# Performance work log

Measured on AMD Instinct MI355X. Metric: run time of the kernel, lower is better.

## Reference

```python
import jax, jax.numpy as jnp
import numpy as np

B, S, D, H = 2, 2048, 1024, 16
DK = D // H


def setup_inputs() -> dict:
    key = jax.random.key(0)
    ks = jax.random.split(key, 7)
    x = jax.random.normal(ks[0], (B, S, D), dtype=jnp.float32)
    gamma = jax.random.normal(ks[1], (D,), dtype=jnp.float32)
    mask = jax.random.randint(ks[2], (B, S), 0, 2, dtype=jnp.int32)
    w_qkv_w = jax.random.normal(ks[3], (D, 3 * D), dtype=jnp.float32) / np.sqrt(D)
    w_qkv_b = jax.random.normal(ks[4], (3 * D,), dtype=jnp.float32) * 0.02
    w_o_w = jax.random.normal(ks[5], (D, D), dtype=jnp.float32) / np.sqrt(D)
    w_o_b = jax.random.normal(ks[6], (D,), dtype=jnp.float32) * 0.02
    return {"x": x, "gamma": gamma, "mask": mask, "w_qkv_w": w_qkv_w,
            "w_qkv_b": w_qkv_b, "w_o_w": w_o_w, "w_o_b": w_o_b}


def reference(x, gamma, mask, w_qkv_w, w_qkv_b, w_o_w, w_o_b):
    b, s, d = x.shape
    # QKV projection, then per-head interleaved chunk (matches torch view+chunk)
    qkv = x @ w_qkv_w + w_qkv_b                      # [B,S,3D]
    qkv = qkv.reshape(b, s, H, 3 * DK).transpose(0, 2, 1, 3)  # [B,H,S,3*dk]
    q, k, v = jnp.split(qkv, 3, axis=-1)             # each [B,H,S,dk]
    scale = 1.0 / np.sqrt(DK).astype(np.float32)
    scores = jnp.einsum('bhqd,bhkd->bhqk', q, k) * scale  # [B,H,S,S]
    m = mask[:, None, None, :]                       # 2D mask -> [B,1,1,S]
    scores = jnp.where(m == 0, -jnp.inf, scores)
    attn = jax.nn.softmax(scores, axis=-1)           # dropout p=0.0 -> identity
    out = jnp.einsum('bhqk,bhkd->bhqd', attn, v)     # [B,H,S,dk]
    out = out.transpose(0, 2, 1, 3).reshape(b, s, d) # [B,S,D]
    out = out @ w_o_w + w_o_b
    return (gamma + 1.0) * out
```

## Files before the change

### kernel.cpp

```cpp
#include <hip/hip_runtime.h>
#include <hip/hip_bf16.h>


using bf16 = __hip_bfloat16;
typedef __attribute__((ext_vector_type(8))) short bf16x8;
typedef __attribute__((ext_vector_type(4))) float f32x4;

#define QSCALE 0.18033688011112042f

static __device__ __forceinline__ f32x4 mfma_bf16(bf16x8 a, bf16x8 b, f32x4 c) {
    return __builtin_amdgcn_mfma_f32_16x16x32_bf16(a, b, c, 0, 0, 0);
}

static __device__ __forceinline__ void gld_lds16(const void* g, void* s) {
    __builtin_amdgcn_global_load_lds(
        (const __attribute__((address_space(1))) unsigned int*)g,
        (__attribute__((address_space(3))) unsigned int*)s,
        16, 0, 0);
}

static __device__ __forceinline__ short f2s(float f) {
    bf16 h = __float2bfloat16(f);
    return *reinterpret_cast<short*>(&h);
}

__global__ void prep_kernel(const float* __restrict__ x, bf16* __restrict__ xb,
                            const float* __restrict__ wqkv, bf16* __restrict__ wqkvT,
                            const float* __restrict__ wo, bf16* __restrict__ woT) {
    __shared__ float tile[32][33];
    int blk = blockIdx.x;
    if (blk < 4096) {
        int i = blk * 256 + threadIdx.x;
        float4 f = reinterpret_cast<const float4*>(x)[i];
        xb[4*i+0] = __float2bfloat16(f.x);
        xb[4*i+1] = __float2bfloat16(f.y);
        xb[4*i+2] = __float2bfloat16(f.z);
        xb[4*i+3] = __float2bfloat16(f.w);
        return;
    }
    const float* in; bf16* out; int R, C, bx, by;
    if (blk < 7168) {
        int idx = blk - 4096; in = wqkv; out = wqkvT; R = 1024; C = 3072;
        bx = idx % 96; by = idx / 96;
    } else {
        int idx = blk - 7168; in = wo; out = woT; R = 1024; C = 1024;
        bx = idx & 31; by = idx >> 5;
    }
    int c0 = bx * 32, r0 = by * 32;
    int xo = threadIdx.x & 31, yo = threadIdx.x >> 5;
#pragma unroll
    for (int i = 0; i < 32; i += 8) tile[yo + i][xo] = in[(size_t)(r0 + yo + i) * C + c0 + xo];
    __syncthreads();
#pragma unroll
    for (int i = 0; i < 32; i += 8)
        out[(size_t)(c0 + yo + i) * R + r0 + xo] = __float2bfloat16(tile[xo][yo + i]);
}

template <int TM, int MINW>
__global__ __launch_bounds__(256, MINW)
void gemm_bt_kernel(const bf16* __restrict__ A, const bf16* __restrict__ Bt,
                    int M, int N, int K,
                    const float* __restrict__ bias,
                    bf16* __restrict__ Qout, bf16* __restrict__ Kout, bf16* __restrict__ Vout) {
    constexpr int MI = TM / 32;
    constexpr int CA = TM / 32;
    __shared__ __align__(16) bf16 As[TM * 64];
    __shared__ __align__(16) bf16 Bs[128 * 64];

    const int tid  = threadIdx.x;
    const int wave = tid >> 6, lane = tid & 63;
    const int quad = lane >> 4, l16 = lane & 15;
    const int wr = wave >> 1, wc = wave & 1;
    const int bm = blockIdx.y, bn = blockIdx.x;

    f32x4 acc[MI][4] = {};

    const int crow = lane >> 3;
    const int sblk = (lane & 7) ^ (crow & 7);
    const bf16* gA[CA]; const bf16* gB[4]; bf16* lA[CA]; bf16* lB[4];
#pragma unroll
    for (int c = 0; c < CA; ++c) {
        int ch = wave * CA + c;
        gA[c] = A + (size_t)(bm * TM + ch * 8 + crow) * K + sblk * 8;
        lA[c] = As + ch * 512 + lane * 8;
    }
#pragma unroll
    for (int c = 0; c < 4; ++c) {
        int ch = wave * 4 + c;
        gB[c] = Bt + (size_t)(bn * 128 + ch * 8 + crow) * K + sblk * 8;
        lB[c] = Bs + ch * 512 + lane * 8;
    }
    const int xr = l16 & 7;

    for (int k0 = 0; k0 < K; k0 += 64) {
#pragma unroll
        for (int c = 0; c < CA; ++c) gld_lds16(gA[c] + k0, lA[c]);
#pragma unroll
        for (int c = 0; c < 4; ++c) gld_lds16(gB[c] + k0, lB[c]);
        __syncthreads();
#pragma unroll
        for (int ks = 0; ks < 2; ++ks) {
            bf16x8 af[MI], bfr[4];
#pragma unroll
            for (int mi = 0; mi < MI; ++mi)
                af[mi] = *(const bf16x8*)(As + (wr * (TM/2) + mi * 16 + l16) * 64 + ((4 * ks + quad) ^ xr) * 8);
#pragma unroll
            for (int ni = 0; ni < 4; ++ni)
                bfr[ni] = *(const bf16x8*)(Bs + (wc * 64 + ni * 16 + l16) * 64 + ((4 * ks + quad) ^ xr) * 8);
#pragma unroll
            for (int mi = 0; mi < MI; ++mi)
#pragma unroll
                for (int ni = 0; ni < 4; ++ni)
                    acc[mi][ni] = mfma_bf16(af[mi], bfr[ni], acc[mi][ni]);
        }
        __syncthreads();
    }

#pragma unroll
    for (int mi = 0; mi < MI; ++mi) {
#pragma unroll
        for (int ni = 0; ni < 4; ++ni) {
            const int col = bn * 128 + wc * 64 + ni * 16 + l16;
            const int row0 = bm * TM + wr * (TM/2) + mi * 16 + quad * 4;
            const float bs = bias[col];
            float vv[4];
#pragma unroll
            for (int r = 0; r < 4; ++r) vv[r] = acc[mi][ni][r] + bs;
            const int h = col / 192;
            const int rr = col - h * 192;
            const int which = rr >> 6, dk = rr & 63;
            const int b = row0 >> 11, s0 = row0 & 2047;
            const size_t bh = (size_t)b * 16 + h;
            if (which == 0) {
#pragma unroll
                for (int r = 0; r < 4; ++r)
                    Qout[(bh * 2048 + s0 + r) * 64 + dk] = __float2bfloat16(vv[r] * QSCALE);
            } else if (which == 1) {
#pragma unroll
                for (int r = 0; r < 4; ++r)
                    Kout[(bh * 2048 + s0 + r) * 64 + dk] = __float2bfloat16(vv[r]);
            } else {
                const int sp0 = (s0 & ~31) | ((s0 & 12) << 1) | ((s0 & 16) >> 2);
                short4 pv;
                pv.x = f2s(vv[0]); pv.y = f2s(vv[1]);
                pv.z = f2s(vv[2]); pv.w = f2s(vv[3]);
                *reinterpret_cast<short4*>(&Vout[(bh * 64 + dk) * 2048 + sp0]) = pv;
            }
        }
    }
}

__global__ __launch_bounds__(512, 2)
void gemm_out_kernel(const bf16* __restrict__ A, const bf16* __restrict__ Bt,
                     const float* __restrict__ bias, const float* __restrict__ gamma,
                     float* __restrict__ Cout) {
    constexpr int K = 1024, N = 1024;
    __shared__ __align__(16) bf16 As[128 * 64];
    __shared__ __align__(16) bf16 Bs[128 * 64];

    const int tid = threadIdx.x;
    const int wave = tid >> 6, lane = tid & 63;
    const int quad = lane >> 4, l16 = lane & 15;
    const int wr = wave >> 1, wc = wave & 1;

    const int lid = blockIdx.x + (blockIdx.y << 3);
    const int w = (lid & 7) * 32 + (lid >> 3);
    const int bm = w >> 3, bn = w & 7;

    f32x4 acc[2][4] = {};

    const int crow = lane >> 3;
    const int sblk = (lane & 7) ^ (crow & 7);
    const bf16* gA[2]; const bf16* gB[2]; bf16* lA[2]; bf16* lB[2];
#pragma unroll
    for (int c = 0; c < 2; ++c) {
        int ch = wave * 2 + c;
        gA[c] = A + (size_t)(bm * 128 + ch * 8 + crow) * K + sblk * 8;
        lA[c] = As + ch * 512 + lane * 8;
        gB[c] = Bt + (size_t)(bn * 128 + ch * 8 + crow) * K + sblk * 8;
        lB[c] = Bs + ch * 512 + lane * 8;
    }
    const int xr = l16 & 7;

    for (int k0 = 0; k0 < K; k0 += 64) {
#pragma unroll
        for (int c = 0; c < 2; ++c) {
            gld_lds16(gA[c] + k0, lA[c]);
            gld_lds16(gB[c] + k0, lB[c]);
        }
        __syncthreads();
#pragma unroll
        for (int ks = 0; ks < 2; ++ks) {
            bf16x8 af[2], bfr[4];
#pragma unroll
            for (int mi = 0; mi < 2; ++mi)
                af[mi] = *(const bf16x8*)(As + (wr * 32 + mi * 16 + l16) * 64 + ((4 * ks + quad) ^ xr) * 8);
#pragma unroll
            for (int ni = 0; ni < 4; ++ni)
                bfr[ni] = *(const bf16x8*)(Bs + (wc * 64 + ni * 16 + l16) * 64 + ((4 * ks + quad) ^ xr) * 8);
#pragma unroll
            for (int mi = 0; mi < 2; ++mi)
#pragma unroll
                for (int ni = 0; ni < 4; ++ni)
                    acc[mi][ni] = mfma_bf16(af[mi], bfr[ni], acc[mi][ni]);
        }
        __syncthreads();
    }

#pragma unroll
    for (int mi = 0; mi < 2; ++mi)
#pragma unroll
        for (int ni = 0; ni < 4; ++ni) {
            const int col = bn * 128 + wc * 64 + ni * 16 + l16;
            const int row0 = bm * 128 + wr * 32 + mi * 16 + quad * 4;
            const float bs = bias[col];
            const float gm = gamma[col] + 1.0f;
#pragma unroll
            for (int r = 0; r < 4; ++r)
                Cout[(size_t)(row0 + r) * N + col] = gm * (acc[mi][ni][r] + bs);
        }
}

__global__ __launch_bounds__(256, 2)
void attn_kernel(const bf16* __restrict__ Qb, const bf16* __restrict__ Kb,
                 const bf16* __restrict__ Vtp, const int* __restrict__ mask,
                 bf16* __restrict__ Aout) {
    __shared__ __align__(16) bf16 Ks[2][2][4096];
    __shared__ __align__(16) bf16 Vs[2][2][4096];
    __shared__ float Biass[2][2][64];

    const int lid = blockIdx.x + (blockIdx.y << 4);
    const int w   = (lid & 7) * 64 + (lid >> 3);
    const int bh  = w >> 4;
    const int b = bh >> 4, h = bh & 15;
    const int q0 = (w & 15) * 128;
    const int tid = threadIdx.x;
    const int wave = tid >> 6, lane = tid & 63;
    const int qg = wave >> 1, kg = wave & 1;
    const int quad = lane >> 4, l16 = lane & 15;
    const int xr = l16 & 7;

    bf16x8 aq[4][2];
#pragma unroll
    for (int m = 0; m < 4; ++m) {
        const bf16* qp = Qb + ((size_t)bh * 2048 + q0 + qg * 64 + m * 16 + l16) * 64;
        aq[m][0] = *(const bf16x8*)(qp + quad * 8);
        aq[m][1] = *(const bf16x8*)(qp + 32 + quad * 8);
    }

    bf16x8 ones;
#pragma unroll
    for (int j = 0; j < 8; ++j) ones[j] = (short)0x3F80;

    f32x4 O[4][4] = {};
    f32x4 Lacc[4] = {};

    const int r8 = lane >> 3, b8 = lane & 7;
    const int srcb = b8 ^ r8;
    const bf16* gK = Kb  + ((size_t)bh * 2048 + wave * 8 + r8) * 64 + srcb * 8;
    const bf16* gV = Vtp + ((size_t)bh * 64 + wave * 8 + r8) * 2048 + srcb * 8;
    const int so = wave * 512 + lane * 8;

    int mreg = 0;
#pragma unroll
    for (int ti = 0; ti < 2; ++ti)
#pragma unroll
        for (int c = 0; c < 2; ++c) {
            gld_lds16(gK + (size_t)ti * 4096 + c * 2048, &Ks[0][ti][c * 2048 + so]);
            gld_lds16(gV + (size_t)ti * 64 + c * 65536, &Vs[0][ti][c * 2048 + so]);
        }
    if (tid < 128) {
        Biass[0][tid >> 6][tid & 63] = mask[b * 2048 + tid] ? -24.0f : -1e30f;
        mreg = mask[b * 2048 + 128 + tid];
    }

    for (int t = 0; t < 16; ++t) {
        __syncthreads();
        const int cur = t & 1, nxt = cur ^ 1;

        if (t < 15) {
            const int u0 = 2 * t + 2;
#pragma unroll
            for (int ti = 0; ti < 2; ++ti)
#pragma unroll
                for (int c = 0; c < 2; ++c) {
                    gld_lds16(gK + (size_t)(u0 + ti) * 4096 + c * 2048, &Ks[nxt][ti][c * 2048 + so]);
                    gld_lds16(gV + (size_t)(u0 + ti) * 64 + c * 65536, &Vs[nxt][ti][c * 2048 + so]);
                }
            if (tid < 128) Biass[nxt][tid >> 6][tid & 63] = mreg ? -24.0f : -1e30f;
        }
        if (t < 14 && tid < 128) mreg = mask[b * 2048 + t * 128 + 256 + tid];

        const bf16* kb = &Ks[cur][kg][0];
        const bf16* vb = &Vs[cur][kg][0];
        f32x4 bias4[4];
        bf16x8 bk[4][2];
#pragma unroll
        for (int kt4 = 0; kt4 < 4; ++kt4) {
            bias4[kt4] = *(const f32x4*)(&Biass[cur][kg][0] + kt4 * 16 + quad * 4);
            const bf16* kp2 = kb + (kt4 * 16 + l16) * 64;
            bk[kt4][0] = *(const bf16x8*)(kp2 + (quad ^ xr) * 8);
            bk[kt4][1] = *(const bf16x8*)(kp2 + ((quad + 4) ^ xr) * 8);
        }
        bf16x8 bv[2][4];
#pragma unroll
        for (int a = 0; a < 2; ++a)
#pragma unroll
            for (int nt = 0; nt < 4; ++nt)
                bv[a][nt] = *(const bf16x8*)(vb + (nt * 16 + l16) * 64 + ((a * 4 + quad) ^ xr) * 8);

        f32x4 sv0[2][4], sv1[2][4];
        __builtin_amdgcn_s_setprio(1);
#pragma unroll
        for (int mm = 0; mm < 2; ++mm)
#pragma unroll
            for (int kt4 = 0; kt4 < 4; ++kt4) {
                f32x4 c = mfma_bf16(bk[kt4][0], aq[mm][0], bias4[kt4]);
                sv0[mm][kt4] = mfma_bf16(bk[kt4][1], aq[mm][1], c);
            }

#pragma unroll
        for (int kt4 = 0; kt4 < 4; ++kt4) {
            f32x4 c0 = mfma_bf16(bk[kt4][0], aq[2][0], bias4[kt4]);
#pragma unroll
            for (int r = 0; r < 4; ++r)
                sv0[0][kt4][r] = __builtin_amdgcn_exp2f(sv0[0][kt4][r]);
            f32x4 c1 = mfma_bf16(bk[kt4][0], aq[3][0], bias4[kt4]);
#pragma unroll
            for (int r = 0; r < 4; ++r)
                sv0[1][kt4][r] = __builtin_amdgcn_exp2f(sv0[1][kt4][r]);
            sv1[0][kt4] = mfma_bf16(bk[kt4][1], aq[2][1], c0);
            sv1[1][kt4] = mfma_bf16(bk[kt4][1], aq[3][1], c1);
        }

#pragma unroll
        for (int mm = 0; mm < 2; ++mm) {
#pragma unroll
            for (int a = 0; a < 2; ++a) {
                bf16x8 pa;
                pa[0] = f2s(sv0[mm][2*a][0]);   pa[1] = f2s(sv0[mm][2*a][1]);
                pa[2] = f2s(sv0[mm][2*a][2]);   pa[3] = f2s(sv0[mm][2*a][3]);
                pa[4] = f2s(sv0[mm][2*a+1][0]); pa[5] = f2s(sv0[mm][2*a+1][1]);
                pa[6] = f2s(sv0[mm][2*a+1][2]); pa[7] = f2s(sv0[mm][2*a+1][3]);
                Lacc[mm] = mfma_bf16(pa, ones, Lacc[mm]);
#pragma unroll
                for (int nt = 0; nt < 4; ++nt)
                    O[mm][nt] = mfma_bf16(pa, bv[a][nt], O[mm][nt]);
#pragma unroll
                for (int r = 0; r < 4; ++r)
                    sv1[mm][2*a + (r >> 1)][(r & 1) + 2*((mm + a) & 1)] =
                        __builtin_amdgcn_exp2f(sv1[mm][2*a + (r >> 1)][(r & 1) + 2*((mm + a) & 1)]);
            }
        }
#pragma unroll
        for (int mm = 0; mm < 2; ++mm)
#pragma unroll
            for (int kt4 = 0; kt4 < 4; ++kt4)
#pragma unroll
                for (int r = 0; r < 4; ++r) {
                    if (((r >> 1) == 0 ? (2*((mm + (kt4 >> 1)) & 1)) : -1) == -1) {}
                }
#pragma unroll
        for (int mm = 0; mm < 2; ++mm)
#pragma unroll
            for (int a = 0; a < 2; ++a)
#pragma unroll
                for (int r = 0; r < 4; ++r) {
                    int kt4 = 2*a + (r >> 1);
                    int ri  = (r & 1) + 2*(((mm + a) & 1) ^ 1);
                    sv1[mm][kt4][ri] = __builtin_amdgcn_exp2f(sv1[mm][kt4][ri]);
                }

#pragma unroll
        for (int mm = 0; mm < 2; ++mm) {
            const int m = 2 + mm;
#pragma unroll
            for (int a = 0; a < 2; ++a) {
                bf16x8 pa;
                pa[0] = f2s(sv1[mm][2*a][0]);   pa[1] = f2s(sv1[mm][2*a][1]);
                pa[2] = f2s(sv1[mm][2*a][2]);   pa[3] = f2s(sv1[mm][2*a][3]);
                pa[4] = f2s(sv1[mm][2*a+1][0]); pa[5] = f2s(sv1[mm][2*a+1][1]);
                pa[6] = f2s(sv1[mm][2*a+1][2]); pa[7] = f2s(sv1[mm][2*a+1][3]);
                Lacc[m] = mfma_bf16(pa, ones, Lacc[m]);
#pragma unroll
                for (int nt = 0; nt < 4; ++nt)
                    O[m][nt] = mfma_bf16(pa, bv[a][nt], O[m][nt]);
            }
        }
        __builtin_amdgcn_s_setprio(0);
    }

    __syncthreads();
    float* cb = (float*)&Ks[0][0][0];
    float* lb = (float*)&Vs[0][0][0];
    if (kg == 1) {
#pragma unroll
        for (int m = 0; m < 4; ++m) {
#pragma unroll
            for (int nt = 0; nt < 4; ++nt)
#pragma unroll
                for (int r = 0; r < 4; ++r)
                    cb[qg * 4096 + (m * 16 + nt * 4 + r) * 64 + lane] = O[m][nt][r];
#pragma unroll
            for (int r = 0; r < 4; ++r)
                lb[qg * 1024 + (m * 4 + r) * 64 + lane] = Lacc[m][r];
        }
    }
    __syncthreads();
    if (kg == 0) {
#pragma unroll
        for (int m = 0; m < 4; ++m) {
            float inv[4];
#pragma unroll
            for (int r = 0; r < 4; ++r)
                inv[r] = __builtin_amdgcn_rcpf(Lacc[m][r] + lb[qg * 1024 + (m * 4 + r) * 64 + lane]);
#pragma unroll
            for (int nt = 0; nt < 4; ++nt)
#pragma unroll
                for (int r = 0; r < 4; ++r) {
                    int row = q0 + qg * 64 + m * 16 + quad * 4 + r;
                    float o = O[m][nt][r] + cb[qg * 4096 + (m * 16 + nt * 4 + r) * 64 + lane];
                    Aout[((size_t)b * 2048 + row) * 1024 + h * 64 + nt * 16 + l16] =
                        __float2bfloat16(o * inv[r]);
                }
        }
    }
}

extern "C" void kernel_launch(void* const* d_in, const int* in_sizes, int n_in,
                              void* d_out, int out_size, void* d_ws, size_t ws_size,
                              hipStream_t stream) {
    const float* x     = (const float*)d_in[0];
    const float* gamma = (const float*)d_in[1];
    const int*   mask  = (const int*)d_in[2];
    const float* wqkv  = (const float*)d_in[3];
    const float* bqkv  = (const float*)d_in[4];
    const float* wo    = (const float*)d_in[5];
    const float* bo    = (const float*)d_in[6];
    float* out = (float*)d_out;

    char* ws = (char*)d_ws;
    const size_t MB = 1u << 20;
    bf16* xb    = (bf16*)(ws);
    bf16* wqkvT = (bf16*)(ws + 8 * MB);
    bf16* woT   = (bf16*)(ws + 14 * MB);
    bf16* Qb    = (bf16*)(ws + 16 * MB);
    bf16* Kb    = (bf16*)(ws + 24 * MB);
    bf16* Vt    = (bf16*)(ws + 32 * MB);
    bf16* attn  = (bf16*)(ws + 40 * MB);

    prep_kernel<<<8192, 256, 0, stream>>>(x, xb, wqkv, wqkvT, wo, woT);

    gemm_bt_kernel<128, 3><<<dim3(24, 32), 256, 0, stream>>>(
        xb, wqkvT, 4096, 3072, 1024, bqkv, Qb, Kb, Vt);

    attn_kernel<<<dim3(16, 32), 256, 0, stream>>>(Qb, Kb, Vt, mask, attn);

    gemm_out_kernel<<<dim3(8, 32), 512, 0, stream>>>(attn, woT, bo, gamma, out);
}
```

Baseline: 180.2 us.

## Software-pipeline second-half softmax exp and PV MFMAs into the next iteration

The exp2, bf16 packing and P·V/row-sum MFMAs for query sub-tiles 2–3 move out of the current key-tile iteration. They now run at the start of the next iteration, interleaved with the QK MFMAs for sub-tiles 0–1, and an epilogue after the loop drains the last tile. This aims to overlap transcendental and conversion work with matrix-core work and cut the serialized tail of each iteration. In exchange, the score fragments and the V fragments must stay in registers across iterations, which raises register pressure and may lower occupancy or cause spills.

```diff
diff --git a/kernel.cpp b/kernel.cpp
--- a/kernel.cpp
+++ b/kernel.cpp
@@ -274,6 +274,9 @@
         mreg = mask[b * 2048 + 128 + tid];
     }
 
+    f32x4 sv1p[2][4];
+    bf16x8 bv[2][4];
+
     for (int t = 0; t < 16; ++t) {
         __syncthreads();
         const int cur = t & 1, nxt = cur ^ 1;
@@ -302,23 +305,56 @@
             bk[kt4][0] = *(const bf16x8*)(kp2 + (quad ^ xr) * 8);
             bk[kt4][1] = *(const bf16x8*)(kp2 + ((quad + 4) ^ xr) * 8);
         }
-        bf16x8 bv[2][4];
+
+        f32x4 sv0[2][4];
+        __builtin_amdgcn_s_setprio(1);
+        if (t > 0) {
+#pragma unroll
+            for (int kt4 = 0; kt4 < 4; ++kt4) {
+                f32x4 c0 = mfma_bf16(bk[kt4][0], aq[0][0], bias4[kt4]);
+#pragma unroll
+                for (int r = 0; r < 4; ++r)
+                    sv1p[0][kt4][r] = __builtin_amdgcn_exp2f(sv1p[0][kt4][r]);
+                f32x4 c1 = mfma_bf16(bk[kt4][0], aq[1][0], bias4[kt4]);
+#pragma unroll
+                for (int r = 0; r < 4; ++r)
+                    sv1p[1][kt4][r] = __builtin_amdgcn_exp2f(sv1p[1][kt4][r]);
+                sv0[0][kt4] = mfma_bf16(bk[kt4][1], aq[0][1], c0);
+                sv0[1][kt4] = mfma_bf16(bk[kt4][1], aq[1][1], c1);
+            }
+#pragma unroll
+            for (int mm = 0; mm < 2; ++mm) {
+#pragma unroll
+                for (int a = 0; a < 2; ++a) {
+                    bf16x8 pa;
+                    pa[0] = f2s(sv1p[mm][2*a][0]);   pa[1] = f2s(sv1p[mm][2*a][1]);
+                    pa[2] = f2s(sv1p[mm][2*a][2]);   pa[3] = f2s(sv1p[mm][2*a][3]);
+                    pa[4] = f2s(sv1p[mm][2*a+1][0]); pa[5] = f2s(sv1p[mm][2*a+1][1]);
+                    pa[6] = f2s(sv1p[mm][2*a+1][2]); pa[7] = f2s(sv1p[mm][2*a+1][3]);
+                    Lacc[2+mm] = mfma_bf16(pa, ones, Lacc[2+mm]);
+#pragma unroll
+                    for (int nt = 0; nt < 4; ++nt)
+                        O[2+mm][nt] = mfma_bf16(pa, bv[a][nt], O[2+mm][nt]);
+                }
+            }
+        } else {
+#pragma unroll
+            for (int kt4 = 0; kt4 < 4; ++kt4) {
+                f32x4 c0 = mfma_bf16(bk[kt4][0], aq[0][0], bias4[kt4]);
+                f32x4 c1 = mfma_bf16(bk[kt4][0], aq[1][0], bias4[kt4]);
+                sv0[0][kt4] = mfma_bf16(bk[kt4][1], aq[0][1], c0);
+                sv0[1][kt4] = mfma_bf16(bk[kt4][1], aq[1][1], c1);
+            }
+        }
+        __builtin_amdgcn_s_setprio(0);
+
 #pragma unroll
         for (int a = 0; a < 2; ++a)
 #pragma unroll
             for (int nt = 0; nt < 4; ++nt)
                 bv[a][nt] = *(const bf16x8*)(vb + (nt * 16 + l16) * 64 + ((a * 4 + quad) ^ xr) * 8);
 
-        f32x4 sv0[2][4], sv1[2][4];
         __builtin_amdgcn_s_setprio(1);
-#pragma unroll
-        for (int mm = 0; mm < 2; ++mm)
-#pragma unroll
-            for (int kt4 = 0; kt4 < 4; ++kt4) {
-                f32x4 c = mfma_bf16(bk[kt4][0], aq[mm][0], bias4[kt4]);
-                sv0[mm][kt4] = mfma_bf16(bk[kt4][1], aq[mm][1], c);
-            }
-
 #pragma unroll
         for (int kt4 = 0; kt4 < 4; ++kt4) {
             f32x4 c0 = mfma_bf16(bk[kt4][0], aq[2][0], bias4[kt4]);
@@ -329,10 +365,9 @@
 #pragma unroll
             for (int r = 0; r < 4; ++r)
                 sv0[1][kt4][r] = __builtin_amdgcn_exp2f(sv0[1][kt4][r]);
-            sv1[0][kt4] = mfma_bf16(bk[kt4][1], aq[2][1], c0);
-            sv1[1][kt4] = mfma_bf16(bk[kt4][1], aq[3][1], c1);
-        }
-
+            sv1p[0][kt4] = mfma_bf16(bk[kt4][1], aq[2][1], c0);
+            sv1p[1][kt4] = mfma_bf16(bk[kt4][1], aq[3][1], c1);
+        }
 #pragma unroll
         for (int mm = 0; mm < 2; ++mm) {
 #pragma unroll
@@ -346,48 +381,32 @@
 #pragma unroll
                 for (int nt = 0; nt < 4; ++nt)
                     O[mm][nt] = mfma_bf16(pa, bv[a][nt], O[mm][nt]);
-#pragma unroll
-                for (int r = 0; r < 4; ++r)
-                    sv1[mm][2*a + (r >> 1)][(r & 1) + 2*((mm + a) & 1)] =
-                        __builtin_amdgcn_exp2f(sv1[mm][2*a + (r >> 1)][(r & 1) + 2*((mm + a) & 1)]);
             }
         }
-#pragma unroll
-        for (int mm = 0; mm < 2; ++mm)
-#pragma unroll
-            for (int kt4 = 0; kt4 < 4; ++kt4)
-#pragma unroll
-                for (int r = 0; r < 4; ++r) {
-                    if (((r >> 1) == 0 ? (2*((mm + (kt4 >> 1)) & 1)) : -1) == -1) {}
-                }
-#pragma unroll
-        for (int mm = 0; mm < 2; ++mm)
-#pragma unroll
-            for (int a = 0; a < 2; ++a)
-#pragma unroll
-                for (int r = 0; r < 4; ++r) {
-                    int kt4 = 2*a + (r >> 1);
-                    int ri  = (r & 1) + 2*(((mm + a) & 1) ^ 1);
-                    sv1[mm][kt4][ri] = __builtin_amdgcn_exp2f(sv1[mm][kt4][ri]);
-                }
-
-#pragma unroll
-        for (int mm = 0; mm < 2; ++mm) {
-            const int m = 2 + mm;
-#pragma unroll
-            for (int a = 0; a < 2; ++a) {
-                bf16x8 pa;
-                pa[0] = f2s(sv1[mm][2*a][0]);   pa[1] = f2s(sv1[mm][2*a][1]);
-                pa[2] = f2s(sv1[mm][2*a][2]);   pa[3] = f2s(sv1[mm][2*a][3]);
-                pa[4] = f2s(sv1[mm][2*a+1][0]); pa[5] = f2s(sv1[mm][2*a+1][1]);
-                pa[6] = f2s(sv1[mm][2*a+1][2]); pa[7] = f2s(sv1[mm][2*a+1][3]);
-                Lacc[m] = mfma_bf16(pa, ones, Lacc[m]);
-#pragma unroll
-                for (int nt = 0; nt < 4; ++nt)
-                    O[m][nt] = mfma_bf16(pa, bv[a][nt], O[m][nt]);
-            }
-        }
         __builtin_amdgcn_s_setprio(0);
+    }
+
+#pragma unroll
+    for (int mm = 0; mm < 2; ++mm)
+#pragma unroll
+        for (int kt4 = 0; kt4 < 4; ++kt4)
+#pragma unroll
+            for (int r = 0; r < 4; ++r)
+                sv1p[mm][kt4][r] = __builtin_amdgcn_exp2f(sv1p[mm][kt4][r]);
+#pragma unroll
+    for (int mm = 0; mm < 2; ++mm) {
+#pragma unroll
+        for (int a = 0; a < 2; ++a) {
+            bf16x8 pa;
+            pa[0] = f2s(sv1p[mm][2*a][0]);   pa[1] = f2s(sv1p[mm][2*a][1]);
+            pa[2] = f2s(sv1p[mm][2*a][2]);   pa[3] = f2s(sv1p[mm][2*a][3]);
+            pa[4] = f2s(sv1p[mm][2*a+1][0]); pa[5] = f2s(sv1p[mm][2*a+1][1]);
+            pa[6] = f2s(sv1p[mm][2*a+1][2]); pa[7] = f2s(sv1p[mm][2*a+1][3]);
+            Lacc[2+mm] = mfma_bf16(pa, ones, Lacc[2+mm]);
+#pragma unroll
+            for (int nt = 0; nt < 4; ++nt)
+                O[2+mm][nt] = mfma_bf16(pa, bv[a][nt], O[2+mm][nt]);
+        }
     }
 
     __syncthreads();
```

Result: slower. 201.8 us (+12.0%).
